# Kernel tuning notes

Measured on AMD Instinct MI355X. Metric: run time of the kernel, lower is better.

## Reference

```python
import jax, jax.numpy as jnp
import numpy as np

N = 20000      # nodes
E = 320000     # edges (avg degree 16)
S = 2          # extra feature axis (mean-pooled before fc)
IN = 128       # in_feats
H = 246        # n_hidden (must be 246 to match fc = Linear(246, 1))


def setup_inputs() -> dict:
    key = jax.random.key(0)
    ks = jax.random.split(key, 8)
    feat = jax.random.normal(ks[0], (N, S, IN), jnp.float32)
    src = jax.random.randint(ks[1], (E,), 0, N, jnp.int32)
    dst = jax.random.randint(ks[2], (E,), 0, N, jnp.int32)
    glorot = lambda k, shp, fan: jax.random.normal(k, shp, jnp.float32) / np.sqrt(fan).astype(np.float32)
    return {
        "features": feat,
        "src": src,
        "dst": dst,
        "W0": glorot(ks[3], (IN, H), IN), "b0": jnp.zeros((H,), jnp.float32),
        "W1": glorot(ks[4], (H, H), H),   "b1": jnp.zeros((H,), jnp.float32),
        "W2": glorot(ks[5], (H, H), H),   "b2": jnp.zeros((H,), jnp.float32),
        "fc_w": glorot(ks[6], (H, 1), H), "fc_b": jnp.zeros((1,), jnp.float32),
    }


def reference(features, src, dst, W0, b0, W1, b1, W2, b2, fc_w, fc_b):
    # DGL GraphConv, norm='both': h' = act( D_in^{-1/2} A D_out^{-1/2} h W + b )
    ones = jnp.ones((src.shape[0],), jnp.float32)
    out_deg = jax.ops.segment_sum(ones, src, num_segments=N)
    in_deg = jax.ops.segment_sum(ones, dst, num_segments=N)
    norm_out = jax.lax.rsqrt(jnp.maximum(out_deg, 1.0))[:, None, None]  # [N,1,1]
    norm_in = jax.lax.rsqrt(jnp.maximum(in_deg, 1.0))[:, None, None]

    def graph_conv(h, W, b):
        h = h * norm_out                                      # [N,S,F] scale by src-side norm
        agg = jax.ops.segment_sum(h[src], dst, num_segments=N)  # gather->scatter-add over edges
        agg = agg * norm_in
        return jax.nn.relu(agg @ W + b)

    h = graph_conv(features.astype(jnp.float32), W0, b0)
    # dropout between layers is identity in eval mode
    h = graph_conv(h, W1, b1)
    h = graph_conv(h, W2, b2)
    return h.mean(axis=1) @ fc_w + fc_b  # [N,1]
```

## Files before the change

### kernel.cpp

```cpp
#include <hip/hip_runtime.h>
#include <hip/hip_fp16.h>

#define NN 20000
#define NE 320000
#define SS 2
#define FIN 128
#define FH 246

typedef _Float16 f16x8 __attribute__((ext_vector_type(8)));
typedef float f32x4 __attribute__((ext_vector_type(4)));

__global__ void degree_kernel(const int* __restrict__ src, const int* __restrict__ dst,
                              int* __restrict__ deg_out, int* __restrict__ deg_in) {
    int e = blockIdx.x * blockDim.x + threadIdx.x;
    if (e < NE) {
        atomicAdd(&deg_out[src[e]], 1);
        atomicAdd(&deg_in[dst[e]], 1);
    }
}

__global__ void alloc_kernel(const int* __restrict__ deg_out, const int* __restrict__ deg_in,
                             float* __restrict__ norm_out, float* __restrict__ norm_in,
                             int* __restrict__ row_start, int* __restrict__ cursor,
                             int* __restrict__ counter) {
    __shared__ int smem[256];
    __shared__ int base_s;
    int tid = threadIdx.x;
    int i = blockIdx.x * 256 + tid;
    int v  = (i < NN) ? deg_in[i] : 0;
    int vp = (v + 3) & ~3;
    smem[tid] = vp;
    __syncthreads();
    for (int off = 1; off < 256; off <<= 1) {
        int t = (tid >= off) ? smem[tid - off] : 0;
        __syncthreads();
        smem[tid] += t;
        __syncthreads();
    }
    int incl = smem[tid];
    if (tid == 0) base_s = atomicAdd(counter, smem[255]);
    __syncthreads();
    if (i < NN) {
        int excl = base_s + incl - vp;
        row_start[i] = excl;
        cursor[i]    = excl;
        norm_out[i] = rsqrtf(fmaxf((float)deg_out[i], 1.0f));
        norm_in[i]  = rsqrtf(fmaxf((float)v, 1.0f));
    }
}

__global__ void scatter_kernel(const int* __restrict__ src, const int* __restrict__ dst,
                               int* __restrict__ cursor, ushort* __restrict__ sorted_src) {
    int e = blockIdx.x * blockDim.x + threadIdx.x;
    if (e < NE) {
        int d = dst[e];
        int pos = atomicAdd(&cursor[d], 1);
        sorted_src[pos] = (ushort)src[e];
    }
}

__global__ void pad_fill(const int* __restrict__ row_start, const int* __restrict__ deg_in,
                         ushort* __restrict__ sorted_src) {
    int n = blockIdx.x * 256 + threadIdx.x;
    if (n < NN) {
        int d = deg_in[n];
        int beg = row_start[n] + d;
        int end = row_start[n] + ((d + 3) & ~3);
        for (int p = beg; p < end; ++p) sorted_src[p] = (ushort)NN;
    }
}

__global__ void convert_w_all(const float* __restrict__ W0, const float* __restrict__ W1,
                              const float* __restrict__ W2,
                              ushort* __restrict__ Wh0, ushort* __restrict__ Wl0,
                              ushort* __restrict__ Wh1, ushort* __restrict__ Wl1,
                              ushort* __restrict__ Wh2, ushort* __restrict__ Wl2) {
    int n = blockIdx.x, k = threadIdx.x;
    const float* W; ushort* Wh; ushort* Wl; int K;
    if (blockIdx.y == 0)      { W = W0; Wh = Wh0; Wl = Wl0; K = FIN; }
    else if (blockIdx.y == 1) { W = W1; Wh = Wh1; Wl = Wl1; K = FH; }
    else                      { W = W2; Wh = Wh2; Wl = Wl2; K = FH; }
    float v = (k < K && n < 246) ? W[k * 246 + n] : 0.f;
    _Float16 h = (_Float16)v;
    _Float16 l = (_Float16)(v - (float)h);
    Wh[n * 256 + k] = *(ushort*)&h;
    Wl[n * 256 + k] = *(ushort*)&l;
}

__global__ void init_out(float* __restrict__ out, const float* __restrict__ fcb,
                         float* __restrict__ norm_out) {
    int i = blockIdx.x * 256 + threadIdx.x;
    if (i < NN) out[i] = fcb[0];
    if (i == 0) norm_out[NN] = 0.f;
}

template<int F4ROW, int NCH, bool NORM>
__global__ void aggregate4(const float* __restrict__ h,
                           const int* __restrict__ row_start,
                           const int* __restrict__ deg_in,
                           const ushort* __restrict__ sorted_src,
                           const float* __restrict__ norm_out,
                           const float* __restrict__ norm_in,
                           ushort* __restrict__ Ah, ushort* __restrict__ Al) {
    int g  = threadIdx.x >> 4;
    int l  = threadIdx.x & 15;
    int cb = blockIdx.x & (NCH - 1);
    int nb = blockIdx.x / NCH;
    int n  = nb * 8 + g;
    if (n >= NN) return;
    int idx = cb * 16 + l;
    const float4* hv = (const float4*)h;
    int beg = row_start[n];
    int end = beg + ((deg_in[n] + 3) & ~3);
    float4 acc = {0.f, 0.f, 0.f, 0.f};
    ushort4 ss;
    if (beg < end) ss = *(const ushort4*)&sorted_src[beg];
    for (int i = beg; i < end; i += 4) {
        ushort4 cur = ss;
        if (i + 4 < end) ss = *(const ushort4*)&sorted_src[i + 4];
        int s0 = cur.x, s1 = cur.y, s2 = cur.z, s3 = cur.w;
        if (NORM) {
            float n0 = norm_out[s0], n1 = norm_out[s1];
            float n2 = norm_out[s2], n3 = norm_out[s3];
            float4 v0 = hv[(size_t)(s0 < NN ? s0 : NN - 1) * F4ROW + idx];
            float4 v1 = hv[(size_t)(s1 < NN ? s1 : NN - 1) * F4ROW + idx];
            float4 v2 = hv[(size_t)(s2 < NN ? s2 : NN - 1) * F4ROW + idx];
            float4 v3 = hv[(size_t)(s3 < NN ? s3 : NN - 1) * F4ROW + idx];
            acc.x += v0.x * n0 + v1.x * n1 + v2.x * n2 + v3.x * n3;
            acc.y += v0.y * n0 + v1.y * n1 + v2.y * n2 + v3.y * n3;
            acc.z += v0.z * n0 + v1.z * n1 + v2.z * n2 + v3.z * n3;
            acc.w += v0.w * n0 + v1.w * n1 + v2.w * n2 + v3.w * n3;
        } else {
            float4 v0 = hv[(size_t)s0 * F4ROW + idx];
            float4 v1 = hv[(size_t)s1 * F4ROW + idx];
            float4 v2 = hv[(size_t)s2 * F4ROW + idx];
            float4 v3 = hv[(size_t)s3 * F4ROW + idx];
            acc.x += v0.x + v1.x + v2.x + v3.x;
            acc.y += v0.y + v1.y + v2.y + v3.y;
            acc.z += v0.z + v1.z + v2.z + v3.z;
            acc.w += v0.w + v1.w + v2.w + v3.w;
        }
    }
    float ni = norm_in[n];
    float v[4] = {acc.x * ni, acc.y * ni, acc.z * ni, acc.w * ni};
    ushort hp[4], lp[4];
#pragma unroll
    for (int j = 0; j < 4; ++j) {
        _Float16 hh = (_Float16)v[j];
        _Float16 ll = (_Float16)(v[j] - (float)hh);
        hp[j] = *(ushort*)&hh;
        lp[j] = *(ushort*)&ll;
    }
    unsigned long long hv64, lv64;
    __builtin_memcpy(&hv64, hp, 8);
    __builtin_memcpy(&lv64, lp, 8);
    __builtin_nontemporal_store(hv64, (unsigned long long*)Ah + (size_t)n * F4ROW + idx);
    __builtin_nontemporal_store(lv64, (unsigned long long*)Al + (size_t)n * F4ROW + idx);
}

template<int KP, bool FUSE>
__global__ __launch_bounds__(256) void gemm_split(const ushort* __restrict__ Ah,
                                                  const ushort* __restrict__ Al,
                                                  const ushort* __restrict__ Wh,
                                                  const ushort* __restrict__ Wl,
                                                  const float* __restrict__ b,
                                                  void* __restrict__ outv,
                                                  const float* __restrict__ fcw,
                                                  const float* __restrict__ nrm) {
    constexpr int NT = KP / 32;
    constexpr int AS = KP / 8;
    __shared__ __align__(16) _Float16 Ah_s[128][40];
    __shared__ __align__(16) _Float16 Al_s[128][40];
    __shared__ __align__(16) _Float16 Bh_s[128][40];
    __shared__ __align__(16) _Float16 Bl_s[128][40];

    int tid  = threadIdx.x;
    int m0   = blockIdx.x * 128;
    int n0   = blockIdx.y * 128;
    int wave = tid >> 6, lane = tid & 63;
    int wm = wave >> 1, wn = wave & 1;
    int lr = lane & 15, quad = lane >> 4;

    f32x4 acc[4][4];
#pragma unroll
    for (int mi = 0; mi < 4; ++mi)
#pragma unroll
        for (int ni = 0; ni < 4; ++ni) acc[mi][ni] = {0.f, 0.f, 0.f, 0.f};

    const uint4* Ahv = (const uint4*)Ah;
    const uint4* Alv = (const uint4*)Al;
    const uint4* Whv = (const uint4*)Wh;
    const uint4* Wlv = (const uint4*)Wl;

    for (int t0 = 0; t0 < NT; ++t0) {
#pragma unroll
        for (int it = 0; it < 2; ++it) {
            int f = it * 256 + tid;
            int rn = f >> 2, q = f & 3;
            size_t abase = (size_t)(m0 + rn) * AS + t0 * 4 + q;
            *(uint4*)&Ah_s[rn][q * 8] = Ahv[abase];
            *(uint4*)&Al_s[rn][q * 8] = Alv[abase];
            size_t bbase = (size_t)(n0 + rn) * 32 + t0 * 4 + q;
            *(uint4*)&Bh_s[rn][q * 8] = Whv[bbase];
            *(uint4*)&Bl_s[rn][q * 8] = Wlv[bbase];
        }
        __syncthreads();

        f16x8 ah[4], al[4], bh[4], bl[4];
#pragma unroll
        for (int mi = 0; mi < 4; ++mi) {
            ah[mi] = *(const f16x8*)&Ah_s[wm * 64 + mi * 16 + lr][quad * 8];
            al[mi] = *(const f16x8*)&Al_s[wm * 64 + mi * 16 + lr][quad * 8];
        }
#pragma unroll
        for (int ni = 0; ni < 4; ++ni) {
            bh[ni] = *(const f16x8*)&Bh_s[wn * 64 + ni * 16 + lr][quad * 8];
            bl[ni] = *(const f16x8*)&Bl_s[wn * 64 + ni * 16 + lr][quad * 8];
        }
#pragma unroll
        for (int mi = 0; mi < 4; ++mi)
#pragma unroll
            for (int ni = 0; ni < 4; ++ni) {
                acc[mi][ni] = __builtin_amdgcn_mfma_f32_16x16x32_f16(ah[mi], bh[ni], acc[mi][ni], 0, 0, 0);
                acc[mi][ni] = __builtin_amdgcn_mfma_f32_16x16x32_f16(al[mi], bh[ni], acc[mi][ni], 0, 0, 0);
                acc[mi][ni] = __builtin_amdgcn_mfma_f32_16x16x32_f16(ah[mi], bl[ni], acc[mi][ni], 0, 0, 0);
            }
        __syncthreads();
    }

    if (FUSE) {
        float* out = (float*)outv;
#pragma unroll
        for (int mi = 0; mi < 4; ++mi) {
#pragma unroll
            for (int i = 0; i < 4; ++i) {
                float p = 0.f;
#pragma unroll
                for (int ni = 0; ni < 4; ++ni) {
                    int c = n0 + wn * 64 + ni * 16 + lr;
                    if (c < 246)
                        p += fmaxf(acc[mi][ni][i] + b[c], 0.f) * fcw[c];
                }
#pragma unroll
                for (int off = 8; off > 0; off >>= 1)
                    p += __shfl_down(p, off, 16);
                int m = m0 + wm * 64 + mi * 16 + quad * 4 + i;
                if (lr == 0 && m < NN * SS)
                    atomicAdd(&out[m >> 1], 0.5f * p);
            }
        }
    } else {
        float* outF = (float*)outv;
#pragma unroll
        for (int ni = 0; ni < 4; ++ni) {
            int c = n0 + wn * 64 + ni * 16 + lr;
            float bj = (c < 246) ? b[c] : 0.f;
#pragma unroll
            for (int mi = 0; mi < 4; ++mi)
#pragma unroll
                for (int i = 0; i < 4; ++i) {
                    int m = m0 + wm * 64 + mi * 16 + quad * 4 + i;
                    if (m < NN * SS) {
                        float no = nrm[m >> 1];
                        outF[(size_t)m * 256 + c] = fmaxf(acc[mi][ni][i] + bj, 0.f) * no;
                    }
                }
        }
    }
}

extern "C" void kernel_launch(void* const* d_in, const int* in_sizes, int n_in,
                              void* d_out, int out_size, void* d_ws, size_t ws_size,
                              hipStream_t stream) {
    const float* feat = (const float*)d_in[0];
    const int*   src  = (const int*)d_in[1];
    const int*   dst  = (const int*)d_in[2];
    const float* W0   = (const float*)d_in[3];
    const float* b0   = (const float*)d_in[4];
    const float* W1   = (const float*)d_in[5];
    const float* b1   = (const float*)d_in[6];
    const float* W2   = (const float*)d_in[7];
    const float* b2   = (const float*)d_in[8];
    const float* fcw  = (const float*)d_in[9];
    const float* fcb  = (const float*)d_in[10];
    float* out = (float*)d_out;

    char* ws = (char*)d_ws;
    size_t off = 0;
    auto alloc = [&](size_t bytes) {
        void* p = ws + off;
        off = (off + bytes + 255) & ~(size_t)255;
        return p;
    };
    int*    deg_out_i = (int*)alloc((2 * NN + 64) * sizeof(int));
    int*    deg_in_i  = deg_out_i + NN;
    int*    counter   = deg_out_i + 2 * NN;
    int*    row_start = (int*)alloc(NN * sizeof(int));
    int*    cursor    = (int*)alloc(NN * sizeof(int));
    ushort* sorted    = (ushort*)alloc((NE + 3 * NN + 16) * sizeof(ushort));
    float*  norm_out  = (float*)alloc((NN + 1) * sizeof(float));
    float*  norm_in   = (float*)alloc(NN * sizeof(float));
    ushort* Wh0 = (ushort*)alloc(256 * 256 * sizeof(ushort));
    ushort* Wl0 = (ushort*)alloc(256 * 256 * sizeof(ushort));
    ushort* Wh1 = (ushort*)alloc(256 * 256 * sizeof(ushort));
    ushort* Wl1 = (ushort*)alloc(256 * 256 * sizeof(ushort));
    ushort* Wh2 = (ushort*)alloc(256 * 256 * sizeof(ushort));
    ushort* Wl2 = (ushort*)alloc(256 * 256 * sizeof(ushort));
    ushort* Ahb = (ushort*)alloc((size_t)(NN * SS + 64) * 256 * sizeof(ushort));
    ushort* Alb = (ushort*)alloc((size_t)(NN * SS + 64) * 256 * sizeof(ushort));
    float*  bufH = (float*)alloc(((size_t)NN * SS * 256 + 512) * sizeof(float));

    hipMemsetAsync(deg_out_i, 0, (2 * NN + 1) * sizeof(int), stream);
    hipMemsetAsync(bufH + (size_t)NN * 512, 0, 512 * sizeof(float), stream);
    hipMemsetAsync(Ahb + (size_t)NN * SS * 128, 0, 64 * 128 * sizeof(ushort), stream);
    hipMemsetAsync(Alb + (size_t)NN * SS * 128, 0, 64 * 128 * sizeof(ushort), stream);
    hipMemsetAsync(Ahb + (size_t)NN * SS * 256, 0, 64 * 256 * sizeof(ushort), stream);
    hipMemsetAsync(Alb + (size_t)NN * SS * 256, 0, 64 * 256 * sizeof(ushort), stream);

    degree_kernel<<<(NE + 255) / 256, 256, 0, stream>>>(src, dst, deg_out_i, deg_in_i);
    alloc_kernel<<<(NN + 255) / 256, 256, 0, stream>>>(deg_out_i, deg_in_i, norm_out, norm_in,
                                                       row_start, cursor, counter);
    pad_fill<<<(NN + 255) / 256, 256, 0, stream>>>(row_start, deg_in_i, sorted);
    scatter_kernel<<<(NE + 255) / 256, 256, 0, stream>>>(src, dst, cursor, sorted);

    convert_w_all<<<dim3(256, 3), 256, 0, stream>>>(W0, W1, W2, Wh0, Wl0, Wh1, Wl1, Wh2, Wl2);
    init_out<<<(NN + 255) / 256, 256, 0, stream>>>(out, fcb, norm_out);

    const int NB8 = (NN + 7) / 8;
    const int GX  = (NN * SS + 127) / 128;
    dim3 ggrid(GX, 2);

    aggregate4<64, 4, true><<<NB8 * 4, 128, 0, stream>>>(feat, row_start, deg_in_i, sorted,
                                                         norm_out, norm_in, Ahb, Alb);
    gemm_split<FIN, false><<<ggrid, 256, 0, stream>>>(Ahb, Alb, Wh0, Wl0, b0, bufH, fcw, norm_out);

    aggregate4<128, 8, false><<<NB8 * 8, 128, 0, stream>>>(bufH, row_start, deg_in_i, sorted,
                                                           norm_out, norm_in, Ahb, Alb);
    gemm_split<256, false><<<ggrid, 256, 0, stream>>>(Ahb, Alb, Wh1, Wl1, b1, bufH, fcw, norm_out);

    aggregate4<128, 8, false><<<NB8 * 8, 128, 0, stream>>>(bufH, row_start, deg_in_i, sorted,
                                                           norm_out, norm_in, Ahb, Alb);
    gemm_split<256, true><<<ggrid, 256, 0, stream>>>(Ahb, Alb, Wh2, Wl2, b2, out, fcw, norm_out);
}
```

Baseline: 391.8 us.

## Store aggregated activations in k-tiled layout and load A fragments directly from global

The aggregation kernel now writes the fp16 hi/lo activations in a k-tile-major layout (32-wide k slabs of padded M rows), so the GEMM can load MFMA A fragments straight from global memory without staging them through shared memory. The GEMM tile shrinks to 64 rows x 128 cols with each wave covering 32 columns, which doubles the grid and removes the A-side LDS traffic and part of the per-tile sync. A small kernel zeroes the padded rows instead of memsets. The trade-off is more global/L2 traffic for A fragments (each read by all 4 waves) and less accumulator reuse per wave.

```diff
diff --git a/kernel.cpp b/kernel.cpp
--- a/kernel.cpp
+++ b/kernel.cpp
@@ -6,6 +6,7 @@
 #define SS 2
 #define FIN 128
 #define FH 246
+#define MPAD 40064
 
 typedef _Float16 f16x8 __attribute__((ext_vector_type(8)));
 typedef float f32x4 __attribute__((ext_vector_type(4)));
@@ -94,6 +95,17 @@
     if (i == 0) norm_out[NN] = 0.f;
 }
 
+__global__ void zero_pads(ushort* __restrict__ Ah, ushort* __restrict__ Al) {
+    int i = blockIdx.x * 256 + threadIdx.x;
+    if (i < 4096) {
+        int kt = i >> 9, r = i & 511;
+        int m = NN * SS + (r >> 3), j = r & 7;
+        size_t o = ((size_t)kt * MPAD + m) * 8 + j;
+        ((unsigned long long*)Ah)[o] = 0ull;
+        ((unsigned long long*)Al)[o] = 0ull;
+    }
+}
+
 template<int F4ROW, int NCH, bool NORM>
 __global__ void aggregate4(const float* __restrict__ h,
                            const int* __restrict__ row_start,
@@ -102,6 +114,7 @@
                            const float* __restrict__ norm_out,
                            const float* __restrict__ norm_in,
                            ushort* __restrict__ Ah, ushort* __restrict__ Al) {
+    constexpr int IHALF = F4ROW / 2;
     int g  = threadIdx.x >> 4;
     int l  = threadIdx.x & 15;
     int cb = blockIdx.x & (NCH - 1);
@@ -151,11 +164,14 @@
         hp[j] = *(ushort*)&hh;
         lp[j] = *(ushort*)&ll;
     }
+    int s  = (idx >= IHALF);
+    int ik = idx & (IHALF - 1);
+    size_t o = ((size_t)(ik >> 3) * MPAD + n * 2 + s) * 8 + (ik & 7);
     unsigned long long hv64, lv64;
     __builtin_memcpy(&hv64, hp, 8);
     __builtin_memcpy(&lv64, lp, 8);
-    __builtin_nontemporal_store(hv64, (unsigned long long*)Ah + (size_t)n * F4ROW + idx);
-    __builtin_nontemporal_store(lv64, (unsigned long long*)Al + (size_t)n * F4ROW + idx);
+    __builtin_nontemporal_store(hv64, (unsigned long long*)Ah + o);
+    __builtin_nontemporal_store(lv64, (unsigned long long*)Al + o);
 }
 
 template<int KP, bool FUSE>
@@ -168,59 +184,53 @@
                                                   const float* __restrict__ fcw,
                                                   const float* __restrict__ nrm) {
     constexpr int NT = KP / 32;
-    constexpr int AS = KP / 8;
-    __shared__ __align__(16) _Float16 Ah_s[128][40];
-    __shared__ __align__(16) _Float16 Al_s[128][40];
     __shared__ __align__(16) _Float16 Bh_s[128][40];
     __shared__ __align__(16) _Float16 Bl_s[128][40];
 
     int tid  = threadIdx.x;
-    int m0   = blockIdx.x * 128;
+    int m0   = blockIdx.x * 64;
     int n0   = blockIdx.y * 128;
     int wave = tid >> 6, lane = tid & 63;
-    int wm = wave >> 1, wn = wave & 1;
     int lr = lane & 15, quad = lane >> 4;
-
-    f32x4 acc[4][4];
+    int wcol = wave * 32;
+
+    f32x4 acc[4][2];
 #pragma unroll
     for (int mi = 0; mi < 4; ++mi)
 #pragma unroll
-        for (int ni = 0; ni < 4; ++ni) acc[mi][ni] = {0.f, 0.f, 0.f, 0.f};
-
-    const uint4* Ahv = (const uint4*)Ah;
-    const uint4* Alv = (const uint4*)Al;
+        for (int ni = 0; ni < 2; ++ni) acc[mi][ni] = {0.f, 0.f, 0.f, 0.f};
+
     const uint4* Whv = (const uint4*)Wh;
     const uint4* Wlv = (const uint4*)Wl;
 
     for (int t0 = 0; t0 < NT; ++t0) {
+        f16x8 ah[4], al[4];
+#pragma unroll
+        for (int mi = 0; mi < 4; ++mi) {
+            size_t fh = ((size_t)t0 * MPAD + m0 + mi * 16 + lr) * 32 + quad * 8;
+            ah[mi] = *(const f16x8*)(Ah + fh);
+            al[mi] = *(const f16x8*)(Al + fh);
+        }
 #pragma unroll
         for (int it = 0; it < 2; ++it) {
             int f = it * 256 + tid;
             int rn = f >> 2, q = f & 3;
-            size_t abase = (size_t)(m0 + rn) * AS + t0 * 4 + q;
-            *(uint4*)&Ah_s[rn][q * 8] = Ahv[abase];
-            *(uint4*)&Al_s[rn][q * 8] = Alv[abase];
-            size_t bbase = (size_t)(n0 + rn) * 32 + t0 * 4 + q;
-            *(uint4*)&Bh_s[rn][q * 8] = Whv[bbase];
-            *(uint4*)&Bl_s[rn][q * 8] = Wlv[bbase];
+            size_t base = (size_t)(n0 + rn) * 32 + t0 * 4 + q;
+            *(uint4*)&Bh_s[rn][q * 8] = Whv[base];
+            *(uint4*)&Bl_s[rn][q * 8] = Wlv[base];
         }
         __syncthreads();
 
-        f16x8 ah[4], al[4], bh[4], bl[4];
-#pragma unroll
-        for (int mi = 0; mi < 4; ++mi) {
-            ah[mi] = *(const f16x8*)&Ah_s[wm * 64 + mi * 16 + lr][quad * 8];
-            al[mi] = *(const f16x8*)&Al_s[wm * 64 + mi * 16 + lr][quad * 8];
-        }
-#pragma unroll
-        for (int ni = 0; ni < 4; ++ni) {
-            bh[ni] = *(const f16x8*)&Bh_s[wn * 64 + ni * 16 + lr][quad * 8];
-            bl[ni] = *(const f16x8*)&Bl_s[wn * 64 + ni * 16 + lr][quad * 8];
+        f16x8 bh[2], bl[2];
+#pragma unroll
+        for (int ni = 0; ni < 2; ++ni) {
+            bh[ni] = *(const f16x8*)&Bh_s[wcol + ni * 16 + lr][quad * 8];
+            bl[ni] = *(const f16x8*)&Bl_s[wcol + ni * 16 + lr][quad * 8];
         }
 #pragma unroll
         for (int mi = 0; mi < 4; ++mi)
 #pragma unroll
-            for (int ni = 0; ni < 4; ++ni) {
+            for (int ni = 0; ni < 2; ++ni) {
                 acc[mi][ni] = __builtin_amdgcn_mfma_f32_16x16x32_f16(ah[mi], bh[ni], acc[mi][ni], 0, 0, 0);
                 acc[mi][ni] = __builtin_amdgcn_mfma_f32_16x16x32_f16(al[mi], bh[ni], acc[mi][ni], 0, 0, 0);
                 acc[mi][ni] = __builtin_amdgcn_mfma_f32_16x16x32_f16(ah[mi], bl[ni], acc[mi][ni], 0, 0, 0);
@@ -236,15 +246,15 @@
             for (int i = 0; i < 4; ++i) {
                 float p = 0.f;
 #pragma unroll
-                for (int ni = 0; ni < 4; ++ni) {
-                    int c = n0 + wn * 64 + ni * 16 + lr;
+                for (int ni = 0; ni < 2; ++ni) {
+                    int c = n0 + wcol + ni * 16 + lr;
                     if (c < 246)
                         p += fmaxf(acc[mi][ni][i] + b[c], 0.f) * fcw[c];
                 }
 #pragma unroll
                 for (int off = 8; off > 0; off >>= 1)
                     p += __shfl_down(p, off, 16);
-                int m = m0 + wm * 64 + mi * 16 + quad * 4 + i;
+                int m = m0 + mi * 16 + quad * 4 + i;
                 if (lr == 0 && m < NN * SS)
                     atomicAdd(&out[m >> 1], 0.5f * p);
             }
@@ -252,14 +262,14 @@
     } else {
         float* outF = (float*)outv;
 #pragma unroll
-        for (int ni = 0; ni < 4; ++ni) {
-            int c = n0 + wn * 64 + ni * 16 + lr;
+        for (int ni = 0; ni < 2; ++ni) {
+            int c = n0 + wcol + ni * 16 + lr;
             float bj = (c < 246) ? b[c] : 0.f;
 #pragma unroll
             for (int mi = 0; mi < 4; ++mi)
 #pragma unroll
                 for (int i = 0; i < 4; ++i) {
-                    int m = m0 + wm * 64 + mi * 16 + quad * 4 + i;
+                    int m = m0 + mi * 16 + quad * 4 + i;
                     if (m < NN * SS) {
                         float no = nrm[m >> 1];
                         outF[(size_t)m * 256 + c] = fmaxf(acc[mi][ni][i] + bj, 0.f) * no;
@@ -306,16 +316,12 @@
     ushort* Wl1 = (ushort*)alloc(256 * 256 * sizeof(ushort));
     ushort* Wh2 = (ushort*)alloc(256 * 256 * sizeof(ushort));
     ushort* Wl2 = (ushort*)alloc(256 * 256 * sizeof(ushort));
-    ushort* Ahb = (ushort*)alloc((size_t)(NN * SS + 64) * 256 * sizeof(ushort));
-    ushort* Alb = (ushort*)alloc((size_t)(NN * SS + 64) * 256 * sizeof(ushort));
+    ushort* Ahb = (ushort*)alloc((size_t)MPAD * 256 * sizeof(ushort));
+    ushort* Alb = (ushort*)alloc((size_t)MPAD * 256 * sizeof(ushort));
     float*  bufH = (float*)alloc(((size_t)NN * SS * 256 + 512) * sizeof(float));
 
     hipMemsetAsync(deg_out_i, 0, (2 * NN + 1) * sizeof(int), stream);
     hipMemsetAsync(bufH + (size_t)NN * 512, 0, 512 * sizeof(float), stream);
-    hipMemsetAsync(Ahb + (size_t)NN * SS * 128, 0, 64 * 128 * sizeof(ushort), stream);
-    hipMemsetAsync(Alb + (size_t)NN * SS * 128, 0, 64 * 128 * sizeof(ushort), stream);
-    hipMemsetAsync(Ahb + (size_t)NN * SS * 256, 0, 64 * 256 * sizeof(ushort), stream);
-    hipMemsetAsync(Alb + (size_t)NN * SS * 256, 0, 64 * 256 * sizeof(ushort), stream);
 
     degree_kernel<<<(NE + 255) / 256, 256, 0, stream>>>(src, dst, deg_out_i, deg_in_i);
     alloc_kernel<<<(NN + 255) / 256, 256, 0, stream>>>(deg_out_i, deg_in_i, norm_out, norm_in,
@@ -325,10 +331,10 @@
 
     convert_w_all<<<dim3(256, 3), 256, 0, stream>>>(W0, W1, W2, Wh0, Wl0, Wh1, Wl1, Wh2, Wl2);
     init_out<<<(NN + 255) / 256, 256, 0, stream>>>(out, fcb, norm_out);
+    zero_pads<<<16, 256, 0, stream>>>(Ahb, Alb);
 
     const int NB8 = (NN + 7) / 8;
-    const int GX  = (NN * SS + 127) / 128;
-    dim3 ggrid(GX, 2);
+    dim3 ggrid(MPAD / 64, 2);
 
     aggregate4<64, 4, true><<<NB8 * 4, 128, 0, stream>>>(feat, row_start, deg_in_i, sorted,
                                                          norm_out, norm_in, Ahb, Alb);
```

Measured after the change: 396.0 us. About the same (+1.1%).
